# Kernel tuning notes

Hardware: AMD Instinct MI355X
Metric: run time of the kernel (lower is better)

The kernel has to match this reference:

```python
import jax, jax.numpy as jnp
import numpy as np

N = 100000   # nodes
E = 1600000  # edges (avg degree 16)
D = 64       # out_channels (in_channels == out_channels, so no zero-padding step)
L = 2        # GatedGraphConv num_layers


def setup_inputs() -> dict:
    key = jax.random.key(0)
    ks = jax.random.split(key, 11)
    w = lambda k, shape: jax.random.normal(k, shape, jnp.float32) * 0.05
    return {
        "x": jax.random.normal(ks[0], (N, D), jnp.float32),
        "edge_index": jax.random.randint(ks[1], (2, E), 0, N, dtype=jnp.int64),
        "conv_w": w(ks[2], (L, D, D)),        # GatedGraphConv per-layer message weight
        "gru_w_ih": w(ks[3], (3 * D, D)),     # GRUCell input->hidden (r|z|n)
        "gru_w_hh": w(ks[4], (3 * D, D)),     # GRUCell hidden->hidden (r|z|n)
        "gru_b_ih": w(ks[5], (3 * D,)),
        "gru_b_hh": w(ks[6], (3 * D,)),
        "lin_w": w(ks[7], (D, D)),            # nn.Linear(out, out)
        "lin_b": w(ks[8], (D,)),
        "attn_w": w(ks[9], (1, D)),           # nn.Linear(out, 1)
        "attn_b": w(ks[10], (1,)),
    }


def reference(x, edge_index, conv_w, gru_w_ih, gru_w_hh, gru_b_ih, gru_b_hh,
              lin_w, lin_b, attn_w, attn_b):
    src, dst = edge_index[0], edge_index[1]
    h = x  # in_channels == out_channels -> no padding
    for i in range(L):
        m = h @ conv_w[i]  # [N, D] transformed messages
        # gather at source nodes, scatter-add into target nodes
        agg = jax.ops.segment_sum(m[src], dst, num_segments=N)  # [N, D]
        # GRUCell(agg, h)
        gi = agg @ gru_w_ih.T + gru_b_ih  # [N, 3D]
        gh = h @ gru_w_hh.T + gru_b_hh    # [N, 3D]
        i_r, i_z, i_n = jnp.split(gi, 3, axis=1)
        h_r, h_z, h_n = jnp.split(gh, 3, axis=1)
        r = jax.nn.sigmoid(i_r + h_r)
        z = jax.nn.sigmoid(i_z + h_z)
        n = jnp.tanh(i_n + r * h_n)
        h = (1.0 - z) * n + z * h
    y = jax.nn.relu(h) @ lin_w.T + lin_b                 # [N, D]
    attn = jax.nn.softmax(y @ attn_w.T + attn_b, axis=0) # [N, 1], softmax over nodes
    return (attn * y).sum(axis=0, keepdims=True)          # [1, D]
```

## Files before the change

kernel.cpp:

```cpp
#include <hip/hip_runtime.h>


typedef __attribute__((ext_vector_type(8))) short s8v;
typedef __attribute__((ext_vector_type(4))) float f32x4;

#define CSR_CAP 12288
#define HSTR 136
#define LSTR 72

__device__ __forceinline__ unsigned short f32_bf16_rn(float x) {
  unsigned u = __float_as_uint(x);
  u += 0x7FFF + ((u >> 16) & 1);
  return (unsigned short)(u >> 16);
}

__device__ __forceinline__ int wave_incl_scan(int v, int lane) {
#pragma unroll
  for (int d = 1; d < 64; d <<= 1) {
    int u = __shfl_up(v, d);
    if (lane >= d) v += u;
  }
  return v;
}

__device__ __forceinline__ int detect_is64(const int* ei, int E) {
  int nz = 0;
  int lim = (E < 512) ? E : 512;
  for (int i = threadIdx.x; i < lim; i += blockDim.x)
    nz |= (ei[2 * i + 1] != 0);
  return __syncthreads_or(nz) ? 0 : 1;
}

__device__ __forceinline__ void load_edge(const int* ei, int E, int is64,
                                          int e, int& s, int& d) {
  if (is64) { s = ei[2 * e]; d = ei[2 * (E + e)]; }
  else      { s = ei[e];     d = ei[E + e]; }
}

__global__ __launch_bounds__(256) void count_kernel(
    const int* __restrict__ ei, int E,
    int* __restrict__ G, int P, int perBlk, int NB) {
  __shared__ int hist[512];
  int tid = threadIdx.x, b = blockIdx.x;
  for (int i = tid; i < 512; i += 256) hist[i] = 0;
  int is64 = detect_is64(ei, E);
  __syncthreads();
  int e0 = b * perBlk, e1 = min(e0 + perBlk, E);
  for (int e = e0 + tid; e < e1; e += 256) {
    int s, d; load_edge(ei, E, is64, e, s, d);
    atomicAdd(&hist[d >> 8], 1);
  }
  __syncthreads();
  for (int i = tid; i < P; i += 256) G[i * NB + b] = hist[i];
}

__global__ __launch_bounds__(256) void scan2a(int* __restrict__ G,
                                              int* __restrict__ total, int NB) {
  __shared__ int wsum[4];
  int p = blockIdx.x, tid = threadIdx.x, lane = tid & 63, wv = tid >> 6;
  int v = G[p * NB + tid];
  int incl = wave_incl_scan(v, lane);
  if (lane == 63) wsum[wv] = incl;
  __syncthreads();
  if (tid == 0) {
    int a = wsum[0], b2 = wsum[1], c = wsum[2], d = wsum[3];
    total[p] = a + b2 + c + d;
    wsum[0] = 0; wsum[1] = a; wsum[2] = a + b2; wsum[3] = a + b2 + c;
  }
  __syncthreads();
  G[p * NB + tid] = incl - v + wsum[wv];
}

__global__ void scan2b(const int* __restrict__ total, int* __restrict__ partStart,
                       int P) {
  int lane = threadIdx.x;
  int running = 0;
  for (int base = 0; base < P; base += 64) {
    int idx = base + lane;
    int v = (idx < P) ? total[idx] : 0;
    int incl = wave_incl_scan(v, lane);
    int tot = __shfl(incl, 63);
    if (idx < P) partStart[idx] = running + incl - v;
    running += tot;
  }
  if (lane == 0) partStart[P] = running;
}

__global__ __launch_bounds__(256) void scatter_kernel(
    const int* __restrict__ ei, int E,
    const int* __restrict__ G, const int* __restrict__ partStart,
    int* __restrict__ bucket, int P, int perBlk, int NB) {
  __shared__ int cur[512];
  int tid = threadIdx.x, b = blockIdx.x;
  int is64 = detect_is64(ei, E);
  for (int i = tid; i < P; i += 256) cur[i] = partStart[i] + G[i * NB + b];
  __syncthreads();
  int e0 = b * perBlk, e1 = min(e0 + perBlk, E);
  for (int e = e0 + tid; e < e1; e += 256) {
    int s, d; load_edge(ei, E, is64, e, s, d);
    int pos = atomicAdd(&cur[d >> 8], 1);
    bucket[pos] = ((d & 255) << 17) | s;
  }
}

__global__ __launch_bounds__(256) void buildcsr_kernel(
    const int* __restrict__ partStart, const int* __restrict__ bucket,
    int* __restrict__ row_ptr, int* __restrict__ col, int N) {
  __shared__ int stage[CSR_CAP];
  __shared__ int hist[256];
  __shared__ int cur[256];
  __shared__ int wsum[4];
  int p = blockIdx.x, tid = threadIdx.x;
  int beg = partStart[p], end = partStart[p + 1];
  int cnt = end - beg;
  int base = p << 8;
  hist[tid] = 0;
  __syncthreads();
  bool staged = (cnt <= CSR_CAP);
  if (staged) {
    for (int i = tid; i < cnt; i += 256) {
      int v = bucket[beg + i];
      stage[i] = v;
      atomicAdd(&hist[(v >> 17) & 255], 1);
    }
  } else {
    for (int i = tid; i < cnt; i += 256)
      atomicAdd(&hist[(bucket[beg + i] >> 17) & 255], 1);
  }
  __syncthreads();
  int lane = tid & 63, wv = tid >> 6;
  int v = hist[tid];
  int incl = wave_incl_scan(v, lane);
  if (lane == 63) wsum[wv] = incl;
  __syncthreads();
  if (tid == 0) {
    int s0 = wsum[0], s1 = wsum[1], s2 = wsum[2];
    wsum[0] = 0; wsum[1] = s0; wsum[2] = s0 + s1; wsum[3] = s0 + s1 + s2;
  }
  __syncthreads();
  int excl = incl - v + wsum[wv];
  cur[tid] = beg + excl;
  if (base + tid < N) {
    if (tid == 0) row_ptr[base] = beg;
    row_ptr[base + tid + 1] = beg + excl + v;
  }
  __syncthreads();
  if (staged) {
    for (int i = tid; i < cnt; i += 256) {
      int v2 = stage[i];
      int pos = atomicAdd(&cur[(v2 >> 17) & 255], 1);
      col[pos] = v2 & 0x1FFFF;
    }
  } else {
    for (int i = tid; i < cnt; i += 256) {
      int v2 = bucket[beg + i];
      int pos = atomicAdd(&cur[(v2 >> 17) & 255], 1);
      col[pos] = v2 & 0x1FFFF;
    }
  }
}

__global__ void wprep_kernel(const float* __restrict__ conv_w,
                             const float* __restrict__ w_ih,
                             const float* __restrict__ whh,
                             const float* __restrict__ lin_w,
                             unsigned short* __restrict__ Bt,
                             unsigned short* __restrict__ Lt) {
  int idx = blockIdx.x * blockDim.x + threadIdx.x;
  if (idx < 65536) {
    int l = idx >> 15;
    int rr = idx & 32767;
    int cp = rr >> 7, p = rr & 127;
    int ch = cp >> 2, g = cp & 3;
    float val = 0.f;
    if (p < 64) {
      int j = (g == 0) ? ch : (g == 1) ? 64 + ch : (g == 2) ? 128 + ch : -1;
      if (j >= 0) {
        const float* C = conv_w + l * 4096 + p * 64;
        const float* W = w_ih + j * 64;
#pragma unroll 8
        for (int k = 0; k < 64; k++) val += C[k] * W[k];
      }
    } else {
      int q = p - 64;
      if (g == 0)      val = whh[ch * 64 + q];
      else if (g == 1) val = whh[(64 + ch) * 64 + q];
      else if (g == 3) val = whh[(128 + ch) * 64 + q];
    }
    Bt[(size_t)l * 32768 + (size_t)cp * 128 + p] = f32_bf16_rn(val);
  } else if (idx < 65536 + 4096) {
    int i2 = idx - 65536;
    float val = lin_w[i2];
    unsigned short hi = f32_bf16_rn(val);
    float fh = __uint_as_float((unsigned)hi << 16);
    unsigned short lo = f32_bf16_rn(val - fh);
    Lt[i2] = hi;
    Lt[4096 + i2] = lo;
  }
}

__global__ __launch_bounds__(256) void cvt16_kernel(
    const float* __restrict__ in, unsigned short* __restrict__ out, int n8) {
  int idx = blockIdx.x * blockDim.x + threadIdx.x;
  if (idx >= n8) return;
  const float4* p = (const float4*)(in + (size_t)idx * 8);
  float4 v0 = p[0], v1 = p[1];
  uint4 o;
  o.x = (unsigned)f32_bf16_rn(v0.x) | ((unsigned)f32_bf16_rn(v0.y) << 16);
  o.y = (unsigned)f32_bf16_rn(v0.z) | ((unsigned)f32_bf16_rn(v0.w) << 16);
  o.z = (unsigned)f32_bf16_rn(v1.x) | ((unsigned)f32_bf16_rn(v1.y) << 16);
  o.w = (unsigned)f32_bf16_rn(v1.z) | ((unsigned)f32_bf16_rn(v1.w) << 16);
  *(uint4*)(out + (size_t)idx * 8) = o;
}

__device__ __forceinline__ void acc_u4(const uint4& r, float* a) {
  a[0] += __uint_as_float(r.x << 16);
  a[1] += __uint_as_float(r.x & 0xFFFF0000u);
  a[2] += __uint_as_float(r.y << 16);
  a[3] += __uint_as_float(r.y & 0xFFFF0000u);
  a[4] += __uint_as_float(r.z << 16);
  a[5] += __uint_as_float(r.z & 0xFFFF0000u);
  a[6] += __uint_as_float(r.w << 16);
  a[7] += __uint_as_float(r.w & 0xFFFF0000u);
}

__global__ __launch_bounds__(512, 4) void gemm_gru_kernel(
    const unsigned short* __restrict__ src16, const int* __restrict__ row_ptr,
    const int* __restrict__ col, const float* __restrict__ hin,
    float* __restrict__ hout, unsigned short* __restrict__ hb16,
    const unsigned short* __restrict__ bt,
    const float* __restrict__ b_ih, const float* __restrict__ b_hh,
    int N, int ntiles, int wb16) {
  __shared__ short Ahi[64 * HSTR];
  __shared__ short Alo[64 * LSTR];
  const int tid = threadIdx.x;
  const int lane = tid & 63, w = tid >> 6;
  const int l15 = lane & 15, ko = (lane >> 4) * 8;

  s8v Bf[2][4];
#pragma unroll
  for (int ct = 0; ct < 2; ct++)
#pragma unroll
    for (int kk = 0; kk < 4; kk++)
      Bf[ct][kk] = *(const s8v*)(bt + (size_t)(32 * w + 16 * ct + l15) * 128 +
                                 kk * 32 + ko);

  const int ch0 = 8 * w + (l15 >> 2);
  const int ch1 = ch0 + 4;
  const float br0 = b_ih[ch0] + b_hh[ch0], br1 = b_ih[ch1] + b_hh[ch1];
  const float bz0 = b_ih[64 + ch0] + b_hh[64 + ch0], bz1 = b_ih[64 + ch1] + b_hh[64 + ch1];
  const float bi0 = b_ih[128 + ch0], bi1 = b_ih[128 + ch1];
  const float bn0 = b_hh[128 + ch0], bn1 = b_hh[128 + ch1];

  const int g = tid >> 3, qc = tid & 7;

  for (int tile = blockIdx.x; tile < ntiles; tile += gridDim.x) {
    const int nb = tile * 64;
    const int node = nb + g;
    {
      float a[8];
#pragma unroll
      for (int i = 0; i < 8; i++) a[i] = 0.f;
      if (node < N) {
        int beg = row_ptr[node], end = row_ptr[node + 1];
        int e = beg;
        for (; e + 4 <= end; e += 4) {
          uint4 r0 = *(const uint4*)(src16 + (size_t)col[e] * 64 + qc * 8);
          uint4 r1 = *(const uint4*)(src16 + (size_t)col[e + 1] * 64 + qc * 8);
          uint4 r2 = *(const uint4*)(src16 + (size_t)col[e + 2] * 64 + qc * 8);
          uint4 r3 = *(const uint4*)(src16 + (size_t)col[e + 3] * 64 + qc * 8);
          acc_u4(r0, a); acc_u4(r1, a); acc_u4(r2, a); acc_u4(r3, a);
        }
        for (; e < end; e++) {
          uint4 r0 = *(const uint4*)(src16 + (size_t)col[e] * 64 + qc * 8);
          acc_u4(r0, a);
        }
      }
      s8v sv;
#pragma unroll
      for (int i = 0; i < 8; i++) sv[i] = (short)f32_bf16_rn(a[i]);
      *(s8v*)&Ahi[g * HSTR + qc * 8] = sv;
    }
    {
      f32x4 v0 = (f32x4)(0.f), v1 = (f32x4)(0.f);
      if (node < N) {
        v0 = *(const f32x4*)(hin + (size_t)node * 64 + qc * 8);
        v1 = *(const f32x4*)(hin + (size_t)node * 64 + qc * 8 + 4);
      }
      s8v hv, lv;
#pragma unroll
      for (int i = 0; i < 8; i++) {
        float x = (i < 4) ? v0[i] : v1[i - 4];
        unsigned short hb = f32_bf16_rn(x);
        hv[i] = (short)hb;
        lv[i] = (short)f32_bf16_rn(x - __uint_as_float((unsigned)hb << 16));
      }
      *(s8v*)&Ahi[g * HSTR + 64 + qc * 8] = hv;
      *(s8v*)&Alo[g * LSTR + qc * 8] = lv;
    }
    __syncthreads();

    f32x4 acc[4][2];
#pragma unroll
    for (int m = 0; m < 4; m++)
#pragma unroll
      for (int ct = 0; ct < 2; ct++) acc[m][ct] = (f32x4)(0.f);

#pragma unroll
    for (int m = 0; m < 4; m++) {
      const short* arh = &Ahi[(16 * m + l15) * HSTR + ko];
      const short* arl = &Alo[(16 * m + l15) * LSTR + ko];
#pragma unroll
      for (int kk = 0; kk < 4; kk++) {
        s8v a_h = *(const s8v*)(arh + kk * 32);
#pragma unroll
        for (int ct = 0; ct < 2; ct++)
          acc[m][ct] = __builtin_amdgcn_mfma_f32_16x16x32_bf16(a_h, Bf[ct][kk], acc[m][ct], 0, 0, 0);
        if (kk >= 2) {
          s8v a_l = *(const s8v*)(arl + (kk - 2) * 32);
#pragma unroll
          for (int ct = 0; ct < 2; ct++)
            acc[m][ct] = __builtin_amdgcn_mfma_f32_16x16x32_bf16(a_l, Bf[ct][kk], acc[m][ct], 0, 0, 0);
        }
      }
    }

    const int srcb = lane & ~3;
#pragma unroll
    for (int m = 0; m < 4; m++) {
#pragma unroll
      for (int ct = 0; ct < 2; ct++) {
#pragma unroll
        for (int gg = 0; gg < 4; gg++) {
          float a = acc[m][ct][gg];
          float r_ = __shfl(a, srcb);
          float z_ = __shfl(a, srcb | 1);
          float i_ = __shfl(a, srcb | 2);
          float hn_ = __shfl(a, srcb | 3);
          if ((lane & 3) == 0) {
            int loc = 16 * m + (lane >> 4) * 4 + gg;
            int nd = nb + loc;
            if (nd < N) {
              int ch = ct ? ch1 : ch0;
              unsigned hi = (unsigned short)Ahi[loc * HSTR + 64 + ch];
              unsigned lo = (unsigned short)Alo[loc * LSTR + ch];
              float hold = __uint_as_float(hi << 16) + __uint_as_float(lo << 16);
              float rr = 1.f / (1.f + __expf(-(r_ + (ct ? br1 : br0))));
              float zz = 1.f / (1.f + __expf(-(z_ + (ct ? bz1 : bz0))));
              float narg = i_ + (ct ? bi1 : bi0) + rr * (hn_ + (ct ? bn1 : bn0));
              narg = fminf(fmaxf(narg, -15.f), 15.f);
              float t = __expf(2.f * narg);
              float nn = (t - 1.f) / (t + 1.f);
              float hv = (1.f - zz) * nn + zz * hold;
              hout[(size_t)nd * 64 + ch] = hv;
              if (wb16) hb16[(size_t)nd * 64 + ch] = f32_bf16_rn(hv);
            }
          }
        }
      }
    }
    __syncthreads();
  }
}

__global__ __launch_bounds__(256, 2) void final_mfma(
    const float* __restrict__ h, const unsigned short* __restrict__ Lt,
    const float* __restrict__ lin_b, const float* __restrict__ attn_w,
    const float* __restrict__ attn_b, float* __restrict__ partials,
    int N, int ntiles) {
  __shared__ short Alds[2 * 64 * 72];
  __shared__ float red[4][64];
  __shared__ float pl[64];
  const int tid = threadIdx.x;
  const int lane = tid & 63, w = tid >> 6;
  const int l15 = lane & 15, ko = (lane >> 4) * 8;
  const int q = lane >> 4;

  s8v Lh[2], Ll[2];
  const int col = 16 * w + l15;
#pragma unroll
  for (int kk = 0; kk < 2; kk++) {
    Lh[kk] = *(const s8v*)(Lt + (size_t)col * 64 + kk * 32 + ko);
    Ll[kk] = *(const s8v*)(Lt + 4096 + (size_t)col * 64 + kk * 32 + ko);
  }
  const float lb = lin_b[col];
  const float aw = attn_w[col];
  const float ab = attn_b[0];
  const int sr = tid >> 2, part = tid & 3;

  float accS = 0.f;
  float accY = 0.f;

  for (int tile = blockIdx.x; tile < ntiles; tile += gridDim.x) {
    const int nb = tile * 64;
    {
      int node = nb + sr;
      f32x4 v[4];
      if (node < N) {
#pragma unroll
        for (int i = 0; i < 4; i++)
          v[i] = *(const f32x4*)(h + (size_t)node * 64 + part * 16 + 4 * i);
      } else {
#pragma unroll
        for (int i = 0; i < 4; i++) v[i] = (f32x4)(0.f);
      }
      short* ah = &Alds[sr * 72 + part * 16];
#pragma unroll
      for (int i2 = 0; i2 < 2; i2++) {
        s8v hv, lv;
#pragma unroll
        for (int e = 0; e < 8; e++) {
          float x = fmaxf(v[i2 * 2 + (e >> 2)][e & 3], 0.f);
          unsigned short hb = f32_bf16_rn(x);
          float fh = __uint_as_float((unsigned)hb << 16);
          unsigned short lo2 = f32_bf16_rn(x - fh);
          hv[e] = (short)hb;
          lv[e] = (short)lo2;
        }
        *(s8v*)(ah + i2 * 8) = hv;
        *(s8v*)(ah + 64 * 72 + i2 * 8) = lv;
      }
    }
    __syncthreads();

    f32x4 acc[4];
#pragma unroll
    for (int m = 0; m < 4; m++) acc[m] = (f32x4)(0.f);
#pragma unroll
    for (int m = 0; m < 4; m++) {
      const short* arow = &Alds[(16 * m + l15) * 72 + ko];
#pragma unroll
      for (int kk = 0; kk < 2; kk++) {
        s8v a_h = *(const s8v*)(arow + kk * 32);
        s8v a_l = *(const s8v*)(arow + 64 * 72 + kk * 32);
        acc[m] = __builtin_amdgcn_mfma_f32_16x16x32_bf16(a_h, Lh[kk], acc[m], 0, 0, 0);
        acc[m] = __builtin_amdgcn_mfma_f32_16x16x32_bf16(a_h, Ll[kk], acc[m], 0, 0, 0);
        acc[m] = __builtin_amdgcn_mfma_f32_16x16x32_bf16(a_l, Lh[kk], acc[m], 0, 0, 0);
      }
    }
    __syncthreads();

    float cc[4][4];
#pragma unroll
    for (int m = 0; m < 4; m++)
#pragma unroll
      for (int g = 0; g < 4; g++) cc[m][g] = (acc[m][g] + lb) * aw;
#pragma unroll
    for (int off = 1; off <= 8; off <<= 1)
#pragma unroll
      for (int m = 0; m < 4; m++)
#pragma unroll
        for (int g = 0; g < 4; g++) cc[m][g] += __shfl_xor(cc[m][g], off);
    if (l15 == 0) {
#pragma unroll
      for (int m = 0; m < 4; m++)
#pragma unroll
        for (int g = 0; g < 4; g++) red[w][16 * m + 4 * q + g] = cc[m][g];
    }
    __syncthreads();
    if (tid < 64) {
      float t = red[0][tid] + red[1][tid] + red[2][tid] + red[3][tid] + ab;
      float p = (nb + tid < N) ? __expf(t) : 0.f;
      pl[tid] = p;
      accS += p;
    }
    __syncthreads();
#pragma unroll
    for (int m = 0; m < 4; m++)
#pragma unroll
      for (int g = 0; g < 4; g++)
        accY += pl[16 * m + 4 * q + g] * (acc[m][g] + lb);
  }

  accY += __shfl_xor(accY, 16);
  accY += __shfl_xor(accY, 32);
  if (lane < 16) partials[(size_t)blockIdx.x * 66 + 16 * w + lane] = accY;
  if (w == 0) {
    float s = accS;
#pragma unroll
    for (int off = 1; off < 64; off <<= 1) s += __shfl_xor(s, off);
    if (lane == 0) partials[(size_t)blockIdx.x * 66 + 64] = s;
  }
}

__global__ void final_p2(const float* __restrict__ partials,
                         float* __restrict__ out, int nb) {
  __shared__ float red[16][65];
  int tid = threadIdx.x;
  int j = tid & 63, grp = tid >> 6;
  float sy = 0.f, ss = 0.f;
  for (int b = grp; b < nb; b += 16) {
    sy += partials[b * 66 + j];
    if (j == 0) ss += partials[b * 66 + 64];
  }
  red[grp][j] = sy;
  if (j == 0) red[grp][64] = ss;
  __syncthreads();
  if (tid < 64) {
    float Y = 0.f, S = 0.f;
#pragma unroll
    for (int i = 0; i < 16; i++) { Y += red[i][tid]; S += red[i][64]; }
    out[tid] = Y / S;
  }
}

extern "C" void kernel_launch(void* const* d_in, const int* in_sizes, int n_in,
                              void* d_out, int out_size, void* d_ws, size_t ws_size,
                              hipStream_t stream) {
  const float* x       = (const float*)d_in[0];
  const int*   ei      = (const int*)d_in[1];
  const float* conv_w  = (const float*)d_in[2];
  const float* gw_ih   = (const float*)d_in[3];
  const float* gw_hh   = (const float*)d_in[4];
  const float* gb_ih   = (const float*)d_in[5];
  const float* gb_hh   = (const float*)d_in[6];
  const float* lin_w   = (const float*)d_in[7];
  const float* lin_b   = (const float*)d_in[8];
  const float* attn_w  = (const float*)d_in[9];
  const float* attn_b  = (const float*)d_in[10];
  float* out = (float*)d_out;

  const int N = in_sizes[0] / 64;
  const int E = in_sizes[1] / 2;
  const int P  = (N + 255) >> 8;
  const int NB = 256;
  const int perBlk = (E + NB - 1) / NB;

  char* ws = (char*)d_ws;
  size_t off = 0;
  auto alloc = [&](size_t bytes) {
    void* p = ws + off;
    off = (off + bytes + 255) & ~(size_t)255;
    return p;
  };
  int*   G         = (int*)alloc((size_t)P * NB * 4);
  int*   total     = (int*)alloc((size_t)P * 4);
  int*   partStart = (int*)alloc((size_t)(P + 1) * 4);
  int*   bucket    = (int*)alloc((size_t)E * 4);
  int*   row_ptr   = (int*)alloc((size_t)(N + 1) * 4);
  int*   colb      = (int*)alloc((size_t)E * 4);
  unsigned short* Bt  = (unsigned short*)alloc(2 * 256 * 128 * 2);
  unsigned short* Lt  = (unsigned short*)alloc(2 * 4096 * 2);
  unsigned short* b16x = (unsigned short*)alloc((size_t)N * 64 * 2);
  unsigned short* b16h = (unsigned short*)alloc((size_t)N * 64 * 2);
  float* hbuf      = (float*)alloc((size_t)N * 64 * 4);
  float* partials  = (float*)alloc(1024 * 66 * 4);
  if (off > ws_size) return;

  count_kernel<<<NB, 256, 0, stream>>>(ei, E, G, P, perBlk, NB);
  scan2a<<<P, 256, 0, stream>>>(G, total, NB);
  scan2b<<<1, 64, 0, stream>>>(total, partStart, P);
  scatter_kernel<<<NB, 256, 0, stream>>>(ei, E, G, partStart, bucket, P, perBlk, NB);
  buildcsr_kernel<<<P, 256, 0, stream>>>(partStart, bucket, row_ptr, colb, N);
  wprep_kernel<<<(65536 + 4096 + 255) / 256, 256, 0, stream>>>(conv_w, gw_ih, gw_hh,
                                                               lin_w, Bt, Lt);
  int n8 = (N * 64) / 8;
  cvt16_kernel<<<(n8 + 255) / 256, 256, 0, stream>>>(x, b16x, n8);

  int ntiles = (N + 63) / 64;
  gemm_gru_kernel<<<512, 512, 0, stream>>>(b16x, row_ptr, colb, x, hbuf, b16h,
                                           Bt, gb_ih, gb_hh, N, ntiles, 1);
  gemm_gru_kernel<<<512, 512, 0, stream>>>(b16h, row_ptr, colb, hbuf, hbuf, b16h,
                                           Bt + 32768, gb_ih, gb_hh, N, ntiles, 0);
  final_mfma<<<512, 256, 0, stream>>>(hbuf, Lt, lin_b, attn_w, attn_b, partials, N, ntiles);
  final_p2<<<1, 1024, 0, stream>>>(partials, out, 512);
}
```

Baseline: 261.3 us.

## Split neighbor aggregation out of GEMM-GRU kernel into a dedicated gather kernel

```diff
diff --git a/kernel.cpp b/kernel.cpp
--- a/kernel.cpp
+++ b/kernel.cpp
@@ -213,20 +213,56 @@
   *(uint4*)(out + (size_t)idx * 8) = o;
 }
 
-__device__ __forceinline__ void acc_u4(const uint4& r, float* a) {
-  a[0] += __uint_as_float(r.x << 16);
-  a[1] += __uint_as_float(r.x & 0xFFFF0000u);
-  a[2] += __uint_as_float(r.y << 16);
-  a[3] += __uint_as_float(r.y & 0xFFFF0000u);
-  a[4] += __uint_as_float(r.z << 16);
-  a[5] += __uint_as_float(r.z & 0xFFFF0000u);
-  a[6] += __uint_as_float(r.w << 16);
-  a[7] += __uint_as_float(r.w & 0xFFFF0000u);
+__global__ __launch_bounds__(256) void gather_kernel(
+    const unsigned short* __restrict__ hb, const int* __restrict__ row_ptr,
+    const int* __restrict__ col, unsigned short* __restrict__ sout, int N) {
+  int gt = blockIdx.x * blockDim.x + threadIdx.x;
+  int n = gt >> 6, lane = gt & 63;
+  if (n >= N) return;
+  int grp = lane >> 4, q = lane & 15;
+  int beg = row_ptr[n], end = row_ptr[n + 1];
+  float4 a0 = make_float4(0.f, 0.f, 0.f, 0.f);
+  float4 a1 = make_float4(0.f, 0.f, 0.f, 0.f);
+  int e = beg + grp;
+  for (; e + 4 < end; e += 8) {
+    int s0 = col[e], s1 = col[e + 4];
+    uint2 r0 = *(const uint2*)(hb + (size_t)s0 * 64 + q * 4);
+    uint2 r1 = *(const uint2*)(hb + (size_t)s1 * 64 + q * 4);
+    a0.x += __uint_as_float(r0.x << 16);
+    a0.y += __uint_as_float(r0.x & 0xFFFF0000u);
+    a0.z += __uint_as_float(r0.y << 16);
+    a0.w += __uint_as_float(r0.y & 0xFFFF0000u);
+    a1.x += __uint_as_float(r1.x << 16);
+    a1.y += __uint_as_float(r1.x & 0xFFFF0000u);
+    a1.z += __uint_as_float(r1.y << 16);
+    a1.w += __uint_as_float(r1.y & 0xFFFF0000u);
+  }
+  if (e < end) {
+    int s0 = col[e];
+    uint2 r0 = *(const uint2*)(hb + (size_t)s0 * 64 + q * 4);
+    a0.x += __uint_as_float(r0.x << 16);
+    a0.y += __uint_as_float(r0.x & 0xFFFF0000u);
+    a0.z += __uint_as_float(r0.y << 16);
+    a0.w += __uint_as_float(r0.y & 0xFFFF0000u);
+  }
+  a0.x += a1.x; a0.y += a1.y; a0.z += a1.z; a0.w += a1.w;
+#pragma unroll
+  for (int off = 16; off <= 32; off <<= 1) {
+    a0.x += __shfl_xor(a0.x, off);
+    a0.y += __shfl_xor(a0.y, off);
+    a0.z += __shfl_xor(a0.z, off);
+    a0.w += __shfl_xor(a0.w, off);
+  }
+  if (grp == 0) {
+    uint2 o;
+    o.x = (unsigned)f32_bf16_rn(a0.x) | ((unsigned)f32_bf16_rn(a0.y) << 16);
+    o.y = (unsigned)f32_bf16_rn(a0.z) | ((unsigned)f32_bf16_rn(a0.w) << 16);
+    *(uint2*)(sout + (size_t)n * 64 + q * 4) = o;
+  }
 }
 
 __global__ __launch_bounds__(512, 4) void gemm_gru_kernel(
-    const unsigned short* __restrict__ src16, const int* __restrict__ row_ptr,
-    const int* __restrict__ col, const float* __restrict__ hin,
+    const unsigned short* __restrict__ s16, const float* __restrict__ hin,
     float* __restrict__ hout, unsigned short* __restrict__ hb16,
     const unsigned short* __restrict__ bt,
     const float* __restrict__ b_ih, const float* __restrict__ b_hh,
@@ -258,28 +294,9 @@
     const int nb = tile * 64;
     const int node = nb + g;
     {
-      float a[8];
-#pragma unroll
-      for (int i = 0; i < 8; i++) a[i] = 0.f;
-      if (node < N) {
-        int beg = row_ptr[node], end = row_ptr[node + 1];
-        int e = beg;
-        for (; e + 4 <= end; e += 4) {
-          uint4 r0 = *(const uint4*)(src16 + (size_t)col[e] * 64 + qc * 8);
-          uint4 r1 = *(const uint4*)(src16 + (size_t)col[e + 1] * 64 + qc * 8);
-          uint4 r2 = *(const uint4*)(src16 + (size_t)col[e + 2] * 64 + qc * 8);
-          uint4 r3 = *(const uint4*)(src16 + (size_t)col[e + 3] * 64 + qc * 8);
-          acc_u4(r0, a); acc_u4(r1, a); acc_u4(r2, a); acc_u4(r3, a);
-        }
-        for (; e < end; e++) {
-          uint4 r0 = *(const uint4*)(src16 + (size_t)col[e] * 64 + qc * 8);
-          acc_u4(r0, a);
-        }
-      }
-      s8v sv;
-#pragma unroll
-      for (int i = 0; i < 8; i++) sv[i] = (short)f32_bf16_rn(a[i]);
-      *(s8v*)&Ahi[g * HSTR + qc * 8] = sv;
+      uint4 sv = make_uint4(0, 0, 0, 0);
+      if (node < N) sv = *(const uint4*)(s16 + (size_t)node * 64 + qc * 8);
+      *(uint4*)&Ahi[g * HSTR + qc * 8] = sv;
     }
     {
       f32x4 v0 = (f32x4)(0.f), v1 = (f32x4)(0.f);
@@ -543,6 +560,7 @@
   unsigned short* Lt  = (unsigned short*)alloc(2 * 4096 * 2);
   unsigned short* b16x = (unsigned short*)alloc((size_t)N * 64 * 2);
   unsigned short* b16h = (unsigned short*)alloc((size_t)N * 64 * 2);
+  unsigned short* s16  = (unsigned short*)alloc((size_t)N * 64 * 2);
   float* hbuf      = (float*)alloc((size_t)N * 64 * 4);
   float* partials  = (float*)alloc(1024 * 66 * 4);
   if (off > ws_size) return;
@@ -557,11 +575,14 @@
   int n8 = (N * 64) / 8;
   cvt16_kernel<<<(n8 + 255) / 256, 256, 0, stream>>>(x, b16x, n8);
 
+  int gb = (N * 64 + 255) / 256;
   int ntiles = (N + 63) / 64;
-  gemm_gru_kernel<<<512, 512, 0, stream>>>(b16x, row_ptr, colb, x, hbuf, b16h,
-                                           Bt, gb_ih, gb_hh, N, ntiles, 1);
-  gemm_gru_kernel<<<512, 512, 0, stream>>>(b16h, row_ptr, colb, hbuf, hbuf, b16h,
-                                           Bt + 32768, gb_ih, gb_hh, N, ntiles, 0);
+  gather_kernel<<<gb, 256, 0, stream>>>(b16x, row_ptr, colb, s16, N);
+  gemm_gru_kernel<<<512, 512, 0, stream>>>(s16, x, hbuf, b16h, Bt,
+                                           gb_ih, gb_hh, N, ntiles, 1);
+  gather_kernel<<<gb, 256, 0, stream>>>(b16h, row_ptr, colb, s16, N);
+  gemm_gru_kernel<<<512, 512, 0, stream>>>(s16, hbuf, hbuf, b16h, Bt + 32768,
+                                           gb_ih, gb_hh, N, ntiles, 0);
   final_mfma<<<512, 256, 0, stream>>>(hbuf, Lt, lin_b, attn_w, attn_b, partials, N, ntiles);
   final_p2<<<1, 1024, 0, stream>>>(partials, out, 512);
 }
```

Measured after the change: 317.0 us. +21.3%, slower.
